# Optimization experiments

Hardware: AMD Instinct MI355X
Metric: run time of the kernel (lower is better)

The kernel has to match this reference:

```python
import jax, jax.numpy as jnp
import numpy as np
from jax import lax

B, T, L, H, K, NL, NB = 32, 512, 2048, 512, 3, 2, 256
PAD = (K - 1) // 2
EPS = 1e-5


def _predictor_params(key):
    k1, k2 = jax.random.split(key)
    s = 1.0 / np.sqrt(H * K).astype(np.float32)
    return dict(
        conv_w=jax.random.normal(k1, (NL, H, H, K), jnp.float32) * s,
        conv_b=jnp.zeros((NL, H), jnp.float32),
        ln_g=jnp.ones((NL, H), jnp.float32),
        ln_b=jnp.zeros((NL, H), jnp.float32),
        lin_w=jax.random.normal(k2, (H, 1), jnp.float32) * 0.02,
        lin_b=jnp.zeros((1,), jnp.float32),
    )


def setup_inputs():
    key = jax.random.key(0)
    ks = jax.random.split(key, 8)
    inp = {
        'x': jax.random.normal(ks[0], (B, T, H), jnp.float32),
        'src_mask': jnp.zeros((B, T), bool),
        'duration_target': jax.random.randint(ks[1], (B, T), 0, 8, jnp.int32),
        'pitch_target': jax.random.normal(ks[2], (B, T), jnp.float32),
        'energy_target': jax.random.uniform(ks[3], (B, T), jnp.float32),
        'max_len': L,
    }
    for name, k in zip(('dur', 'pit', 'en'), ks[4:7]):
        for p, v in _predictor_params(k).items():
            inp[name + '_' + p] = v
    inp['pitch_bins'] = jnp.linspace(-3.0, 3.0, NB - 1)
    inp['energy_bins'] = jnp.linspace(0.0, 1.0, NB - 1)
    k1, k2 = jax.random.split(ks[7])
    inp['pitch_emb'] = jax.random.normal(k1, (NB, H), jnp.float32) * 0.02
    inp['energy_emb'] = jax.random.normal(k2, (NB, H), jnp.float32) * 0.02
    return inp


def _layer_norm(h, g, b):
    m = jnp.mean(h, -1, keepdims=True)
    v = jnp.var(h, -1, keepdims=True)
    return (h - m) * lax.rsqrt(v + EPS) * g + b


def _predictor(x, cw, cb, lg, lb, lw, lbias, mask):
    # stack of [Conv1d(k=3,same) -> ReLU -> LayerNorm] x NL, then Linear -> 1
    out = x
    for i in range(NL):
        h = lax.conv_general_dilated(out.transpose(0, 2, 1), cw[i], (1,), [(PAD, PAD)],
                                     dimension_numbers=('NCH', 'OIH', 'NCH'))
        h = h.transpose(0, 2, 1) + cb[i]  # [B, T, H]
        out = _layer_norm(jax.nn.relu(h), lg[i], lb[i])
    out = (out @ lw)[..., 0] + lbias[0]  # [B, T]
    return jnp.where(mask, 0.0, out)


def _length_regulate(x, duration, max_len):
    # vectorized equivalent of the per-token expand+concat+pad loop
    csum = jnp.cumsum(duration, axis=1)                     # [B, T]
    frames = jnp.arange(max_len)                            # [L]
    idx = jax.vmap(lambda c: jnp.searchsorted(c, frames, side='right'))(csum)  # [B, L]
    idx = jnp.clip(idx, 0, x.shape[1] - 1)
    out = jnp.take_along_axis(x, idx[:, :, None], axis=1)   # [B, L, H]
    mel_len = jnp.minimum(csum[:, -1], max_len)             # [B]
    out = out * (frames[None, :] < mel_len[:, None])[..., None]
    return out, mel_len


def reference(x, src_mask, duration_target, pitch_target, energy_target, max_len,
              dur_conv_w, dur_conv_b, dur_ln_g, dur_ln_b, dur_lin_w, dur_lin_b,
              pit_conv_w, pit_conv_b, pit_ln_g, pit_ln_b, pit_lin_w, pit_lin_b,
              en_conv_w, en_conv_b, en_ln_g, en_ln_b, en_lin_w, en_lin_b,
              pitch_bins, energy_bins, pitch_emb, energy_emb):
    log_d = _predictor(x, dur_conv_w, dur_conv_b, dur_ln_g, dur_ln_b, dur_lin_w, dur_lin_b, src_mask)
    pitch_pred = _predictor(x, pit_conv_w, pit_conv_b, pit_ln_g, pit_ln_b, pit_lin_w, pit_lin_b, src_mask)
    energy_pred = _predictor(x, en_conv_w, en_conv_b, en_ln_g, en_ln_b, en_lin_w, en_lin_b, src_mask)
    # torch.bucketize(target, bins) (right=False) == searchsorted side='left'
    p_emb = pitch_emb[jnp.searchsorted(pitch_bins, pitch_target, side='left')]
    e_emb = energy_emb[jnp.searchsorted(energy_bins, energy_target, side='left')]
    x2 = x + p_emb + e_emb
    out, mel_len = _length_regulate(x2, duration_target, max_len)
    return (out, pitch_pred, energy_pred, log_d, mel_len)
```

## Files before the change

kernel.cpp:

```cpp
#include <hip/hip_runtime.h>
#include <hip/hip_bf16.h>

#define B_ 32
#define T_ 512
#define TP_ 514
#define L_ 2048
#define H_ 512
#define NRR (B_*T_)
#define KC_ 1536
#define NB_ 256
#define EPS_ 1e-5f
#define XPE ((size_t)B_ * TP_ * H_)

typedef __bf16 bf16;
typedef __bf16 bf16x8 __attribute__((ext_vector_type(8)));
typedef float f32x4 __attribute__((ext_vector_type(4)));

static const size_t WC_BYTES  = (size_t)6 * H_ * KC_ * 2;
static const size_t XP_BYTES  = XPE * 2;
static const size_t Y_BYTES   = (size_t)3 * NRR * H_ * 2;

__device__ __forceinline__ void gload16(const void* g, void* l) {
    __builtin_amdgcn_global_load_lds(
        (const __attribute__((address_space(1))) unsigned int*)g,
        (__attribute__((address_space(3))) unsigned int*)l, 16, 0, 0);
}

__global__ void k_prep_wc(const float* __restrict__ wd, const float* __restrict__ wp,
                          const float* __restrict__ we, bf16* __restrict__ wc) {
    int e = blockIdx.x * 256 + threadIdx.x;
    if (e >= 6 * H_ * KC_) return;
    int m   = e / (H_ * KC_);
    int rem = e % (H_ * KC_);
    int o  = rem / KC_;
    int r2 = rem % KC_;
    int k  = r2 / H_;
    int c  = r2 % H_;
    int p = m >> 1, i = m & 1;
    const float* w = (p == 0) ? wd : (p == 1 ? wp : we);
    float v = w[((size_t)i * H_ * H_ + (size_t)o * H_ + c) * 3 + k];
    wc[e] = (bf16)v;
}

__global__ void k_pad(const float* __restrict__ x, bf16* __restrict__ xp0,
                      bf16* __restrict__ xp1) {
    int wid = threadIdx.x >> 6, lane = threadIdx.x & 63;
    int row = blockIdx.x * 4 + wid;
    int b = row / TP_, tp = row % TP_;
    bf16* d0 = xp0 + (size_t)row * H_ + lane * 8;
    if (tp == 0 || tp == TP_ - 1) {
        bf16x8 z;
#pragma unroll
        for (int i = 0; i < 8; ++i) z[i] = (bf16)0.0f;
        *(bf16x8*)d0 = z;
#pragma unroll
        for (int p = 0; p < 3; ++p)
            *(bf16x8*)(xp1 + p * XPE + (size_t)row * H_ + lane * 8) = z;
    } else {
        const f32x4* p = (const f32x4*)(x + ((size_t)(b * T_ + tp - 1)) * H_ + lane * 8);
        f32x4 u = p[0], v = p[1];
        bf16x8 o;
        o[0] = (bf16)u[0]; o[1] = (bf16)u[1]; o[2] = (bf16)u[2]; o[3] = (bf16)u[3];
        o[4] = (bf16)v[0]; o[5] = (bf16)v[1]; o[6] = (bf16)v[2]; o[7] = (bf16)v[3];
        *(bf16x8*)d0 = o;
    }
}

__global__ void k_buckets(const float* __restrict__ pt, const float* __restrict__ et,
                          const float* __restrict__ pbins, const float* __restrict__ ebins,
                          int* __restrict__ pidx, int* __restrict__ eidx) {
    int r = blockIdx.x * 256 + threadIdx.x;
    if (r >= NRR) return;
    {
        float v = pt[r];
        int lo = 0, hi = NB_ - 1;
        while (lo < hi) { int mid = (lo + hi) >> 1; if (pbins[mid] < v) lo = mid + 1; else hi = mid; }
        pidx[r] = lo;
    }
    {
        float v = et[r];
        int lo = 0, hi = NB_ - 1;
        while (lo < hi) { int mid = (lo + hi) >> 1; if (ebins[mid] < v) lo = mid + 1; else hi = mid; }
        eidx[r] = lo;
    }
}

__global__ void k_scan(const int* __restrict__ dur, int* __restrict__ csum,
                       float* __restrict__ mel_out) {
    int b = blockIdx.x, t = threadIdx.x;
    __shared__ int s[T_];
    s[t] = dur[b * T_ + t];
    __syncthreads();
    for (int off = 1; off < T_; off <<= 1) {
        int v = (t >= off) ? s[t - off] : 0;
        __syncthreads();
        s[t] += v;
        __syncthreads();
    }
    csum[b * T_ + t] = s[t];
    if (t == T_ - 1) mel_out[b] = (float)((s[t] < L_) ? s[t] : L_);
}

__global__ void k_gather(const float* __restrict__ x, const float* __restrict__ pemb,
                         const float* __restrict__ eemb, const int* __restrict__ pidx,
                         const int* __restrict__ eidx, const int* __restrict__ csum,
                         float* __restrict__ out) {
    int bi = blockIdx.x;
    int b  = bi >> 9;
    int l0 = (bi & 511) << 2;
    __shared__ int cs[T_];
    cs[threadIdx.x]       = csum[b * T_ + threadIdx.x];
    cs[threadIdx.x + 256] = csum[b * T_ + threadIdx.x + 256];
    __syncthreads();
    int wid = threadIdx.x >> 6, lane = threadIdx.x & 63;
    int l = l0 + wid;
    int mel = cs[T_ - 1]; if (mel > L_) mel = L_;
    float* op = out + ((size_t)(b * L_ + l)) * H_ + lane * 8;
    if (l >= mel) {
        f32x4 z = {0.f, 0.f, 0.f, 0.f};
        ((f32x4*)op)[0] = z;
        ((f32x4*)op)[1] = z;
        return;
    }
    int lo = 0, hi = T_;
    while (lo < hi) { int mid = (lo + hi) >> 1; if (cs[mid] <= l) lo = mid + 1; else hi = mid; }
    int idx = (lo < T_ - 1) ? lo : (T_ - 1);
    int rr = b * T_ + idx;
    int pi = pidx[rr], ei = eidx[rr];
    const f32x4* xp = (const f32x4*)(x    + (size_t)rr * H_ + lane * 8);
    const f32x4* pp = (const f32x4*)(pemb + (size_t)pi * H_ + lane * 8);
    const f32x4* ep = (const f32x4*)(eemb + (size_t)ei * H_ + lane * 8);
    ((f32x4*)op)[0] = xp[0] + pp[0] + ep[0];
    ((f32x4*)op)[1] = xp[1] + pp[1] + ep[1];
}

template<int LAYER>
__global__ void k_gemm(const bf16* __restrict__ Xp, const bf16* __restrict__ Wall,
                       const float* __restrict__ cb0, const float* __restrict__ cb1,
                       const float* __restrict__ cb2, bf16* __restrict__ Y) {
    __shared__ bf16 lA[128 * 64];
    __shared__ bf16 lB[128 * 64];
    int p, oBase;
    const bf16* A;
    const bf16* W;
    if constexpr (LAYER == 0) {
        int cB = blockIdx.x * 128;
        p = cB >> 9; oBase = cB & 511;
        A = Xp;
        W = Wall + ((size_t)(2 * p) * H_ + oBase) * KC_;
    } else {
        p = blockIdx.z; oBase = blockIdx.x * 128;
        A = Xp + (size_t)p * XPE;
        W = Wall + ((size_t)(2 * p + 1) * H_ + oBase) * KC_;
    }
    const float* cbp  = (p == 0) ? cb0 : (p == 1 ? cb1 : cb2);
    const float* bias = cbp + (LAYER ? H_ : 0);

    int tid = threadIdx.x;
    int wid = tid >> 6, lane = tid & 63;
    int wr = wid >> 1, wc = wid & 1;
    int rowBase = blockIdx.y * 128;
    int b  = rowBase >> 9;
    int t0 = rowBase & (T_ - 1);

    f32x4 acc[4][4];
#pragma unroll
    for (int m = 0; m < 4; ++m)
#pragma unroll
        for (int n = 0; n < 4; ++n) acc[m][n] = (f32x4){0.f, 0.f, 0.f, 0.f};

    int lr = lane & 15, kq = lane >> 4;
    int rsub = lane >> 3, csub = (lane & 7) << 3;

    for (int step = 0; step < 24; ++step) {
        int k  = step >> 3;
        int c0 = (step & 7) << 6;
        const bf16* srcA = A + ((size_t)(b * TP_ + t0 + k)) * H_ + c0;
        const bf16* srcB = W + step * 64;
#pragma unroll
        for (int q = 0; q < 4; ++q) {
            int r0 = (wid * 4 + q) * 8;
            gload16(srcA + (size_t)(r0 + rsub) * H_  + csub, &lA[r0 * 64]);
            gload16(srcB + (size_t)(r0 + rsub) * KC_ + csub, &lB[r0 * 64]);
        }
        __syncthreads();
#pragma unroll
        for (int kk = 0; kk < 64; kk += 32) {
            bf16x8 af[4], bfr[4];
#pragma unroll
            for (int m = 0; m < 4; ++m)
                af[m] = *(const bf16x8*)&lA[(wr * 64 + m * 16 + lr) * 64 + kk + kq * 8];
#pragma unroll
            for (int n = 0; n < 4; ++n)
                bfr[n] = *(const bf16x8*)&lB[(wc * 64 + n * 16 + lr) * 64 + kk + kq * 8];
#pragma unroll
            for (int m = 0; m < 4; ++m)
#pragma unroll
                for (int n = 0; n < 4; ++n)
                    acc[m][n] = __builtin_amdgcn_mfma_f32_16x16x32_bf16(af[m], bfr[n], acc[m][n], 0, 0, 0);
        }
        __syncthreads();
    }

#pragma unroll
    for (int n = 0; n < 4; ++n) {
        int o = oBase + wc * 64 + n * 16 + lr;
        float bi = bias[o];
#pragma unroll
        for (int m = 0; m < 4; ++m) {
            int row = rowBase + wr * 64 + m * 16 + 4 * kq;
#pragma unroll
            for (int r = 0; r < 4; ++r)
                Y[((size_t)p * NRR + row + r) * H_ + o] = (bf16)fmaxf(acc[m][n][r] + bi, 0.f);
        }
    }
}

__global__ void k_ln_store(const bf16* __restrict__ Yin,
                           const float* __restrict__ g0, const float* __restrict__ g1,
                           const float* __restrict__ g2,
                           const float* __restrict__ bb0, const float* __restrict__ bb1,
                           const float* __restrict__ bb2, bf16* __restrict__ xp1) {
    int wid = threadIdx.x >> 6, lane = threadIdx.x & 63;
    int rg = blockIdx.x * 4 + wid;
    int p = rg >> 14, r = rg & (NRR - 1);
    const float* g   = (p == 0) ? g0 : (p == 1 ? g1 : g2);
    const float* bta = (p == 0) ? bb0 : (p == 1 ? bb1 : bb2);
    bf16x8 a = *(const bf16x8*)(Yin + ((size_t)p * NRR + r) * H_ + lane * 8);
    float f[8];
#pragma unroll
    for (int i = 0; i < 8; ++i) f[i] = (float)a[i];
    float s1 = 0.f, s2 = 0.f;
#pragma unroll
    for (int i = 0; i < 8; ++i) { s1 += f[i]; s2 += f[i] * f[i]; }
    for (int m = 1; m < 64; m <<= 1) { s1 += __shfl_xor(s1, m); s2 += __shfl_xor(s2, m); }
    float mean = s1 * (1.f / H_);
    float var  = s2 * (1.f / H_) - mean * mean;
    float rs   = rsqrtf(var + EPS_);
    const f32x4* gp = (const f32x4*)g;
    const f32x4* bp = (const f32x4*)bta;
    f32x4 ga = gp[lane * 2], gb = gp[lane * 2 + 1];
    f32x4 ba = bp[lane * 2], bbv = bp[lane * 2 + 1];
    bf16x8 o;
    o[0] = (bf16)((f[0] - mean) * rs * ga[0] + ba[0]);
    o[1] = (bf16)((f[1] - mean) * rs * ga[1] + ba[1]);
    o[2] = (bf16)((f[2] - mean) * rs * ga[2] + ba[2]);
    o[3] = (bf16)((f[3] - mean) * rs * ga[3] + ba[3]);
    o[4] = (bf16)((f[4] - mean) * rs * gb[0] + bbv[0]);
    o[5] = (bf16)((f[5] - mean) * rs * gb[1] + bbv[1]);
    o[6] = (bf16)((f[6] - mean) * rs * gb[2] + bbv[2]);
    o[7] = (bf16)((f[7] - mean) * rs * gb[3] + bbv[3]);
    int bb = r >> 9, t = r & (T_ - 1);
    *(bf16x8*)(xp1 + (size_t)p * XPE + ((size_t)(bb * TP_ + t + 1)) * H_ + lane * 8) = o;
}

__global__ void k_ln_linear(const bf16* __restrict__ Yin,
                            const float* __restrict__ g0, const float* __restrict__ g1,
                            const float* __restrict__ g2,
                            const float* __restrict__ bb0, const float* __restrict__ bb1,
                            const float* __restrict__ bb2,
                            const float* __restrict__ w0p, const float* __restrict__ w1p,
                            const float* __restrict__ w2p,
                            const float* __restrict__ lb0, const float* __restrict__ lb1,
                            const float* __restrict__ lb2,
                            const unsigned char* __restrict__ mask,
                            float* __restrict__ o0, float* __restrict__ o1,
                            float* __restrict__ o2) {
    int wid = threadIdx.x >> 6, lane = threadIdx.x & 63;
    int rg = blockIdx.x * 4 + wid;
    int p = rg >> 14, r = rg & (NRR - 1);
    const float* g   = ((p == 0) ? g0 : (p == 1 ? g1 : g2)) + H_;
    const float* bta = ((p == 0) ? bb0 : (p == 1 ? bb1 : bb2)) + H_;
    const float* lw  = (p == 0) ? w0p : (p == 1 ? w1p : w2p);
    const float* lb  = (p == 0) ? lb0 : (p == 1 ? lb1 : lb2);
    float*       op  = (p == 0) ? o0 : (p == 1 ? o1 : o2);
    bf16x8 a = *(const bf16x8*)(Yin + ((size_t)p * NRR + r) * H_ + lane * 8);
    float f[8];
#pragma unroll
    for (int i = 0; i < 8; ++i) f[i] = (float)a[i];
    float s1 = 0.f, s2 = 0.f;
#pragma unroll
    for (int i = 0; i < 8; ++i) { s1 += f[i]; s2 += f[i] * f[i]; }
    for (int m = 1; m < 64; m <<= 1) { s1 += __shfl_xor(s1, m); s2 += __shfl_xor(s2, m); }
    float mean = s1 * (1.f / H_);
    float var  = s2 * (1.f / H_) - mean * mean;
    float rs   = rsqrtf(var + EPS_);
    const f32x4* gp = (const f32x4*)g;
    const f32x4* bp = (const f32x4*)bta;
    const f32x4* wp = (const f32x4*)lw;
    f32x4 ga = gp[lane * 2], gb = gp[lane * 2 + 1];
    f32x4 ba = bp[lane * 2], bbv = bp[lane * 2 + 1];
    f32x4 wa = wp[lane * 2], wb = wp[lane * 2 + 1];
    float s = ((f[0] - mean) * rs * ga[0] + ba[0]) * wa[0]
            + ((f[1] - mean) * rs * ga[1] + ba[1]) * wa[1]
            + ((f[2] - mean) * rs * ga[2] + ba[2]) * wa[2]
            + ((f[3] - mean) * rs * ga[3] + ba[3]) * wa[3]
            + ((f[4] - mean) * rs * gb[0] + bbv[0]) * wb[0]
            + ((f[5] - mean) * rs * gb[1] + bbv[1]) * wb[1]
            + ((f[6] - mean) * rs * gb[2] + bbv[2]) * wb[2]
            + ((f[7] - mean) * rs * gb[3] + bbv[3]) * wb[3];
    for (int m = 1; m < 64; m <<= 1) s += __shfl_xor(s, m);
    if (lane == 0) op[r] = mask[r] ? 0.f : (s + lb[0]);
}

extern "C" void kernel_launch(void* const* d_in, const int* in_sizes, int n_in,
                              void* d_out, int out_size, void* d_ws, size_t ws_size,
                              hipStream_t stream) {
    const float* x  = (const float*)d_in[0];
    const unsigned char* mask = (const unsigned char*)d_in[1];
    const int*   dur = (const int*)d_in[2];
    const float* pt  = (const float*)d_in[3];
    const float* et  = (const float*)d_in[4];
    const float* cw[3]    = {(const float*)d_in[6],  (const float*)d_in[12], (const float*)d_in[18]};
    const float* cb[3]    = {(const float*)d_in[7],  (const float*)d_in[13], (const float*)d_in[19]};
    const float* lg[3]    = {(const float*)d_in[8],  (const float*)d_in[14], (const float*)d_in[20]};
    const float* lbn[3]   = {(const float*)d_in[9],  (const float*)d_in[15], (const float*)d_in[21]};
    const float* lw[3]    = {(const float*)d_in[10], (const float*)d_in[16], (const float*)d_in[22]};
    const float* lbias[3] = {(const float*)d_in[11], (const float*)d_in[17], (const float*)d_in[23]};
    const float* pbins = (const float*)d_in[24];
    const float* ebins = (const float*)d_in[25];
    const float* pemb  = (const float*)d_in[26];
    const float* eemb  = (const float*)d_in[27];

    float* out0 = (float*)d_out;
    const size_t OUT0 = (size_t)B_ * L_ * H_;
    float* pitch_out  = out0 + OUT0;
    float* energy_out = pitch_out + NRR;
    float* logd_out   = energy_out + NRR;
    float* mel_out    = logd_out + NRR;

    char* ws = (char*)d_ws;
    bf16*  wc   = (bf16*)ws;
    bf16*  xp0  = (bf16*)(ws + WC_BYTES);
    bf16*  xp1  = (bf16*)(ws + WC_BYTES + XP_BYTES);
    bf16*  y    = (bf16*)(ws + WC_BYTES + 4 * XP_BYTES);
    int*   csum = (int*)(ws + WC_BYTES + 4 * XP_BYTES + Y_BYTES);
    int*   pidx = csum + NRR;
    int*   eidx = pidx + NRR;

    k_prep_wc<<<(6 * H_ * KC_ + 255) / 256, 256, 0, stream>>>(cw[0], cw[1], cw[2], wc);
    k_pad<<<B_ * TP_ / 4, 256, 0, stream>>>(x, xp0, xp1);
    k_buckets<<<(NRR + 255) / 256, 256, 0, stream>>>(pt, et, pbins, ebins, pidx, eidx);
    k_scan<<<B_, T_, 0, stream>>>(dur, csum, mel_out);
    k_gather<<<B_ * L_ / 4, 256, 0, stream>>>(x, pemb, eemb, pidx, eidx, csum, out0);

    dim3 g0(12, 128);
    k_gemm<0><<<g0, 256, 0, stream>>>(xp0, wc, cb[0], cb[1], cb[2], y);
    k_ln_store<<<3 * NRR / 4, 256, 0, stream>>>(y, lg[0], lg[1], lg[2],
                                                lbn[0], lbn[1], lbn[2], xp1);
    dim3 g1(4, 128, 3);
    k_gemm<1><<<g1, 256, 0, stream>>>(xp1, wc, cb[0], cb[1], cb[2], y);
    k_ln_linear<<<3 * NRR / 4, 256, 0, stream>>>(y, lg[0], lg[1], lg[2],
                                                 lbn[0], lbn[1], lbn[2],
                                                 lw[0], lw[1], lw[2],
                                                 lbias[0], lbias[1], lbias[2],
                                                 mask, logd_out, pitch_out, energy_out);
}
```

Baseline: 302.2 us.

## Enlarge GEMM tiles to 128x256 with swizzled LDS and fuse bucketize into gather

The conv GEMM now uses 512-thread blocks computing 128x256 output tiles, with an XOR-swizzled LDS layout to reduce bank conflicts and a flat, swizzled block order for cache locality. The bucketize kernel is removed; gather performs the bin search itself using bins cached in LDS. This aims to raise operand reuse in the dominant GEMMs and drop a launch and an index round trip. It trades this for more LDS per block, possibly lower occupancy, and redundant per-frame bin searches.

```diff
diff --git a/kernel.cpp b/kernel.cpp
--- a/kernel.cpp
+++ b/kernel.cpp
@@ -66,25 +66,6 @@
     }
 }
 
-__global__ void k_buckets(const float* __restrict__ pt, const float* __restrict__ et,
-                          const float* __restrict__ pbins, const float* __restrict__ ebins,
-                          int* __restrict__ pidx, int* __restrict__ eidx) {
-    int r = blockIdx.x * 256 + threadIdx.x;
-    if (r >= NRR) return;
-    {
-        float v = pt[r];
-        int lo = 0, hi = NB_ - 1;
-        while (lo < hi) { int mid = (lo + hi) >> 1; if (pbins[mid] < v) lo = mid + 1; else hi = mid; }
-        pidx[r] = lo;
-    }
-    {
-        float v = et[r];
-        int lo = 0, hi = NB_ - 1;
-        while (lo < hi) { int mid = (lo + hi) >> 1; if (ebins[mid] < v) lo = mid + 1; else hi = mid; }
-        eidx[r] = lo;
-    }
-}
-
 __global__ void k_scan(const int* __restrict__ dur, int* __restrict__ csum,
                        float* __restrict__ mel_out) {
     int b = blockIdx.x, t = threadIdx.x;
@@ -102,15 +83,21 @@
 }
 
 __global__ void k_gather(const float* __restrict__ x, const float* __restrict__ pemb,
-                         const float* __restrict__ eemb, const int* __restrict__ pidx,
-                         const int* __restrict__ eidx, const int* __restrict__ csum,
+                         const float* __restrict__ eemb, const float* __restrict__ pt,
+                         const float* __restrict__ et, const float* __restrict__ pbins,
+                         const float* __restrict__ ebins, const int* __restrict__ csum,
                          float* __restrict__ out) {
     int bi = blockIdx.x;
     int b  = bi >> 9;
     int l0 = (bi & 511) << 2;
     __shared__ int cs[T_];
+    __shared__ float pb[NB_ - 1], eb[NB_ - 1];
     cs[threadIdx.x]       = csum[b * T_ + threadIdx.x];
     cs[threadIdx.x + 256] = csum[b * T_ + threadIdx.x + 256];
+    if (threadIdx.x < NB_ - 1) {
+        pb[threadIdx.x] = pbins[threadIdx.x];
+        eb[threadIdx.x] = ebins[threadIdx.x];
+    }
     __syncthreads();
     int wid = threadIdx.x >> 6, lane = threadIdx.x & 63;
     int l = l0 + wid;
@@ -126,7 +113,10 @@
     while (lo < hi) { int mid = (lo + hi) >> 1; if (cs[mid] <= l) lo = mid + 1; else hi = mid; }
     int idx = (lo < T_ - 1) ? lo : (T_ - 1);
     int rr = b * T_ + idx;
-    int pi = pidx[rr], ei = eidx[rr];
+    float pv = pt[rr], ev = et[rr];
+    int pi, ei;
+    { int a = 0, c = NB_ - 1; while (a < c) { int mid = (a + c) >> 1; if (pb[mid] < pv) a = mid + 1; else c = mid; } pi = a; }
+    { int a = 0, c = NB_ - 1; while (a < c) { int mid = (a + c) >> 1; if (eb[mid] < ev) a = mid + 1; else c = mid; } ei = a; }
     const f32x4* xp = (const f32x4*)(x    + (size_t)rr * H_ + lane * 8);
     const f32x4* pp = (const f32x4*)(pemb + (size_t)pi * H_ + lane * 8);
     const f32x4* ep = (const f32x4*)(eemb + (size_t)ei * H_ + lane * 8);
@@ -135,42 +125,39 @@
 }
 
 template<int LAYER>
-__global__ void k_gemm(const bf16* __restrict__ Xp, const bf16* __restrict__ Wall,
-                       const float* __restrict__ cb0, const float* __restrict__ cb1,
-                       const float* __restrict__ cb2, bf16* __restrict__ Y) {
+__global__ __launch_bounds__(512)
+void k_gemm(const bf16* __restrict__ Xp, const bf16* __restrict__ Wall,
+            const float* __restrict__ cb0, const float* __restrict__ cb1,
+            const float* __restrict__ cb2, bf16* __restrict__ Y) {
     __shared__ bf16 lA[128 * 64];
-    __shared__ bf16 lB[128 * 64];
-    int p, oBase;
-    const bf16* A;
-    const bf16* W;
-    if constexpr (LAYER == 0) {
-        int cB = blockIdx.x * 128;
-        p = cB >> 9; oBase = cB & 511;
-        A = Xp;
-        W = Wall + ((size_t)(2 * p) * H_ + oBase) * KC_;
-    } else {
-        p = blockIdx.z; oBase = blockIdx.x * 128;
-        A = Xp + (size_t)p * XPE;
-        W = Wall + ((size_t)(2 * p + 1) * H_ + oBase) * KC_;
-    }
+    __shared__ bf16 lB[256 * 64];
+
+    int bid = blockIdx.x;
+    int swz = (bid & 7) * 96 + (bid >> 3);
+    int rowblk = swz / 6, colblk = swz % 6;
+    int p  = colblk >> 1;
+    int oB = (colblk & 1) * 256;
+    int rowBase = rowblk * 128;
+
+    const bf16* A = (LAYER == 0) ? Xp : (Xp + (size_t)p * XPE);
+    const bf16* W = Wall + ((size_t)(2 * p + LAYER) * H_ + oB) * KC_;
     const float* cbp  = (p == 0) ? cb0 : (p == 1 ? cb1 : cb2);
-    const float* bias = cbp + (LAYER ? H_ : 0);
+    const float* bias = cbp + LAYER * H_;
 
     int tid = threadIdx.x;
     int wid = tid >> 6, lane = tid & 63;
-    int wr = wid >> 1, wc = wid & 1;
-    int rowBase = blockIdx.y * 128;
-    int b  = rowBase >> 9;
-    int t0 = rowBase & (T_ - 1);
+    int wr = wid >> 2, wc = wid & 3;
+    int lr = lane & 15, kq = lane >> 4;
+    int xr = lr & 7;
+    int rsub = lane >> 3;
+    int csw  = ((lane & 7) ^ rsub) << 3;
+    int b = rowBase >> 9, t0 = rowBase & (T_ - 1);
 
     f32x4 acc[4][4];
 #pragma unroll
     for (int m = 0; m < 4; ++m)
 #pragma unroll
         for (int n = 0; n < 4; ++n) acc[m][n] = (f32x4){0.f, 0.f, 0.f, 0.f};
-
-    int lr = lane & 15, kq = lane >> 4;
-    int rsub = lane >> 3, csub = (lane & 7) << 3;
 
     for (int step = 0; step < 24; ++step) {
         int k  = step >> 3;
@@ -178,21 +165,26 @@
         const bf16* srcA = A + ((size_t)(b * TP_ + t0 + k)) * H_ + c0;
         const bf16* srcB = W + step * 64;
 #pragma unroll
+        for (int q = 0; q < 2; ++q) {
+            int r0 = (wid * 2 + q) * 8;
+            gload16(srcA + (size_t)(r0 + rsub) * H_ + csw, lA + r0 * 64);
+        }
+#pragma unroll
         for (int q = 0; q < 4; ++q) {
             int r0 = (wid * 4 + q) * 8;
-            gload16(srcA + (size_t)(r0 + rsub) * H_  + csub, &lA[r0 * 64]);
-            gload16(srcB + (size_t)(r0 + rsub) * KC_ + csub, &lB[r0 * 64]);
+            gload16(srcB + (size_t)(r0 + rsub) * KC_ + csw, lB + r0 * 64);
         }
         __syncthreads();
 #pragma unroll
         for (int kk = 0; kk < 64; kk += 32) {
+            int co = ((((kk >> 3) + kq) ^ xr)) << 3;
             bf16x8 af[4], bfr[4];
 #pragma unroll
             for (int m = 0; m < 4; ++m)
-                af[m] = *(const bf16x8*)&lA[(wr * 64 + m * 16 + lr) * 64 + kk + kq * 8];
+                af[m] = *(const bf16x8*)&lA[(wr * 64 + m * 16 + lr) * 64 + co];
 #pragma unroll
             for (int n = 0; n < 4; ++n)
-                bfr[n] = *(const bf16x8*)&lB[(wc * 64 + n * 16 + lr) * 64 + kk + kq * 8];
+                bfr[n] = *(const bf16x8*)&lB[(wc * 64 + n * 16 + lr) * 64 + co];
 #pragma unroll
             for (int m = 0; m < 4; ++m)
 #pragma unroll
@@ -204,7 +196,7 @@
 
 #pragma unroll
     for (int n = 0; n < 4; ++n) {
-        int o = oBase + wc * 64 + n * 16 + lr;
+        int o = oB + wc * 64 + n * 16 + lr;
         float bi = bias[o];
 #pragma unroll
         for (int m = 0; m < 4; ++m) {
@@ -335,21 +327,16 @@
     bf16*  xp1  = (bf16*)(ws + WC_BYTES + XP_BYTES);
     bf16*  y    = (bf16*)(ws + WC_BYTES + 4 * XP_BYTES);
     int*   csum = (int*)(ws + WC_BYTES + 4 * XP_BYTES + Y_BYTES);
-    int*   pidx = csum + NRR;
-    int*   eidx = pidx + NRR;
 
     k_prep_wc<<<(6 * H_ * KC_ + 255) / 256, 256, 0, stream>>>(cw[0], cw[1], cw[2], wc);
     k_pad<<<B_ * TP_ / 4, 256, 0, stream>>>(x, xp0, xp1);
-    k_buckets<<<(NRR + 255) / 256, 256, 0, stream>>>(pt, et, pbins, ebins, pidx, eidx);
     k_scan<<<B_, T_, 0, stream>>>(dur, csum, mel_out);
-    k_gather<<<B_ * L_ / 4, 256, 0, stream>>>(x, pemb, eemb, pidx, eidx, csum, out0);
-
-    dim3 g0(12, 128);
-    k_gemm<0><<<g0, 256, 0, stream>>>(xp0, wc, cb[0], cb[1], cb[2], y);
+    k_gather<<<B_ * L_ / 4, 256, 0, stream>>>(x, pemb, eemb, pt, et, pbins, ebins, csum, out0);
+
+    k_gemm<0><<<768, 512, 0, stream>>>(xp0, wc, cb[0], cb[1], cb[2], y);
     k_ln_store<<<3 * NRR / 4, 256, 0, stream>>>(y, lg[0], lg[1], lg[2],
                                                 lbn[0], lbn[1], lbn[2], xp1);
-    dim3 g1(4, 128, 3);
-    k_gemm<1><<<g1, 256, 0, stream>>>(xp1, wc, cb[0], cb[1], cb[2], y);
+    k_gemm<1><<<768, 512, 0, stream>>>(xp1, wc, cb[0], cb[1], cb[2], y);
     k_ln_linear<<<3 * NRR / 4, 256, 0, stream>>>(y, lg[0], lg[1], lg[2],
                                                  lbn[0], lbn[1], lbn[2],
                                                  lw[0], lw[1], lw[2],
```

Measured after the change: 274.0 us. 1.1x faster.
